# Performance work log

Hardware: AMD Instinct MI355X
Metric: run time of the kernel (lower is better)

The kernel has to match this reference:

```python
import jax, jax.numpy as jnp
import numpy as np

GAMMA = 2          # relu(cos_sim)**gamma, from init gamma=2
EPS = 1e-8         # torch CosineSimilarity eps (norm clamp)
B, C, H, WID = 4, 256, 64, 64


def setup_inputs() -> dict:
    key = jax.random.key(0)
    kx, kw = jax.random.split(key)
    x = jax.random.normal(kx, (B, C, H, WID), dtype=jnp.float32)
    # 1x1 conv (nlayers=1): weight [C_out, C_in], bias [C_out]
    W = jax.random.normal(kw, (C, C), dtype=jnp.float32) * 0.02
    b = jnp.zeros((C,), dtype=jnp.float32)
    return {"x": x, "W": W, "b": b}


def reference(x, W, b):
    # x: [B,C,H,W]. Flatten pixels: p/q index (h*W+w).
    Bs, Cs, Hs, Ws = x.shape
    xf = x.reshape(Bs, Cs, Hs * Ws)                      # [B,C,P]
    norm = jnp.sqrt(jnp.sum(xf * xf, axis=1, keepdims=True))
    xn = xf / jnp.maximum(norm, EPS)                     # channel-normalized
    # full pairwise cosine similarity over pixels, relu, power gamma
    s = jax.nn.relu(jnp.einsum('bcp,bcq->bpq', xn, xn)) ** GAMMA  # [B,P,Q]
    # transform: 1x1 conv = per-pixel linear map over channels
    gx = jnp.einsum('oc,bcp->bop', W, xf) + b[None, :, None]      # [B,C,P]
    # y[b,c,p] = sum_q s[b,p,q] * gx[b,c,q]  (== 'bijhw,bchw->bcij')
    y = jnp.einsum('bpq,bcq->bcp', s, gx)
    return y.reshape(Bs, Cs, Hs, Ws)
```

## Files before the change

kernel.cpp:

```cpp
#include <hip/hip_runtime.h>

#define BN 4
#define CN 256
#define PN 4096
#define QT 64
#define TSTR 264

typedef __attribute__((ext_vector_type(8))) short short8;
typedef __attribute__((ext_vector_type(8))) unsigned short ushort8;
typedef __attribute__((ext_vector_type(4))) float f32x4;
typedef __attribute__((ext_vector_type(2))) unsigned int u32x2;
typedef unsigned int u32;

__device__ __forceinline__ unsigned short f2bf(float f) {
  u32 u = __builtin_bit_cast(u32, f);
  return (unsigned short)((u + 0x7fffu + ((u >> 16) & 1u)) >> 16);
}

__device__ __forceinline__ void async_copy16(const void* g, void* l) {
  __builtin_amdgcn_global_load_lds((const __attribute__((address_space(1))) u32*)g,
                                   (__attribute__((address_space(3))) u32*)l, 16, 0, 0);
}

__global__ __launch_bounds__(256) void k_nx(const float* __restrict__ x,
                                            float* __restrict__ mnorm,
                                            unsigned short* __restrict__ xnT) {
  __shared__ unsigned short tl[64 * TSTR];
  __shared__ float red[4][64];
  const int b = blockIdx.y, p0 = blockIdx.x * 64;
  const int tid = threadIdx.x;
  const int tp = tid & 63, cg = tid >> 6;
  const float* xp = x + ((size_t)b * CN + cg * 64) * PN + p0 + tp;
  float v[64];
  float ss = 0.f;
#pragma unroll
  for (int i = 0; i < 64; ++i) {
    v[i] = xp[(size_t)i * PN];
    ss += v[i] * v[i];
  }
  red[cg][tp] = ss;
  __syncthreads();
  float nrm = sqrtf(red[0][tp] + red[1][tp] + red[2][tp] + red[3][tp]);
  float mn = fmaxf(nrm, 1e-8f);
  float rn = 1.f / mn;
  if (cg == 0) mnorm[b * PN + p0 + tp] = mn;
  unsigned int* tl32 = (unsigned int*)tl;
#pragma unroll
  for (int j = 0; j < 32; ++j) {
    unsigned int w = (unsigned int)f2bf(v[2 * j] * rn) |
                     ((unsigned int)f2bf(v[2 * j + 1] * rn) << 16);
    tl32[tp * (TSTR / 2) + cg * 32 + j] = w;
  }
  __syncthreads();
  unsigned short* xd = xnT + ((size_t)b * PN + p0) * CN;
  const int row = tid >> 2, qc = tid & 3;
#pragma unroll
  for (int i = 0; i < 8; ++i) {
    ushort8 o = *(const ushort8*)(tl + row * TSTR + i * 32 + qc * 8);
    *(ushort8*)(xd + (size_t)row * CN + i * 32 + qc * 8) = o;
  }
}

__global__ void k_gx(const float* __restrict__ Wm, const float* __restrict__ bias,
                     const unsigned short* __restrict__ xnT, const float* __restrict__ mnorm,
                     unsigned short* __restrict__ gxv) {
  int b = blockIdx.z;
  int m0 = blockIdx.y * 64;
  int q0 = blockIdx.x * 64;
  int tid = threadIdx.x;
  int wave = tid >> 6, lane = tid & 63;
  int lr = lane & 15, g = lane >> 4;

  short8 af[8];
  {
    const float* wr = Wm + (size_t)(m0 + wave * 16 + lr) * CN;
#pragma unroll
    for (int k = 0; k < 8; ++k) {
      const float* ap = wr + k * 32 + g * 8;
      short8 a;
#pragma unroll
      for (int j = 0; j < 8; ++j) a[j] = (short)f2bf(ap[j]);
      af[k] = a;
    }
  }
  f32x4 acc[4];
#pragma unroll
  for (int n = 0; n < 4; ++n) acc[n] = (f32x4){0.f, 0.f, 0.f, 0.f};

  const unsigned short* xb = xnT + (size_t)b * PN * CN;
#pragma unroll
  for (int n = 0; n < 4; ++n) {
    const unsigned short* bp = xb + (size_t)(q0 + n * 16 + lr) * CN + g * 8;
#pragma unroll
    for (int k = 0; k < 8; ++k) {
      short8 bf = *(const short8*)(bp + k * 32);
      acc[n] = __builtin_amdgcn_mfma_f32_16x16x32_bf16(af[k], bf, acc[n], 0, 0, 0);
    }
  }
#pragma unroll
  for (int n = 0; n < 4; ++n) {
    int q = q0 + n * 16 + lr;
    float mn = mnorm[b * PN + q];
#pragma unroll
    for (int i = 0; i < 4; ++i) {
      int c = m0 + wave * 16 + g * 4 + i;
      float v = acc[n][i] * mn + bias[c];
      gxv[((size_t)b * CN + c) * PN + q] = f2bf(v);
    }
  }
}

extern __shared__ char smem[];

__global__ __launch_bounds__(512, 2) void k_attn(const unsigned short* __restrict__ xnT,
                                                 const unsigned short* __restrict__ gxv,
                                                 float* __restrict__ d0, float* __restrict__ d1,
                                                 float* __restrict__ d2, float* __restrict__ d3,
                                                 int lq, int ntiles) {
  const int fid = blockIdx.x;
  const int b = fid & 3;
  const int qs = (fid >> 2) & ((1 << lq) - 1);
  const int pblk = fid >> (2 + lq);
  const int tid = threadIdx.x;
  const int wave = tid >> 6, lane = tid & 63, lr = lane & 15, g = lane >> 4;
  const int qbase = qs * (PN >> lq);
  const int p0 = pblk * 256 + wave * 32;
  float* dst = (qs == 0) ? d0 : (qs == 1) ? d1 : (qs == 2) ? d2 : d3;

  const char* xbc = (const char*)xnT + (size_t)b * PN * 512;
  const char* vbc = (const char*)gxv + (size_t)b * CN * PN * 2;

  const int kofs = (lane & 15) * 512 + (lane >> 4) * 16 + wave * 64;
  const int vofs = wave * 131072 + (lane & 15) * 8192 + (lane >> 4) * 16;
  const int ldst = tid * 16;
  const int lane16 = lane * 16;
  const int swb = lr * 16 + (g >> 1) * 256 + (g & 1) * 8;

  auto issue_K = [&](int t) {
    char* kb = smem + (t & 1) * 65536;
    const char* kg = xbc + (size_t)(qbase + t * QT) * 512 + kofs;
#pragma unroll
    for (int j = 0; j < 4; ++j) async_copy16(kg + j * 8192, kb + ldst + j * 8192);
  };
  auto issue_V = [&](int t) {
    char* vb = smem + (t & 1) * 65536 + 32768;
    const char* vg = vbc + (size_t)(qbase + t * QT) * 2 + vofs;
    async_copy16(vg, vb + ldst);
    async_copy16(vg + 1048576, vb + ldst + 8192);
    async_copy16(vg + 64, vb + ldst + 16384);
    async_copy16(vg + 1048576 + 64, vb + ldst + 24576);
  };

  issue_K(0);
  issue_V(0);

  short8 qf[2][8];
#pragma unroll
  for (int mt = 0; mt < 2; ++mt) {
    const char* qp = xbc + (size_t)(p0 + mt * 16 + lr) * 512 + g * 16;
#pragma unroll
    for (int k = 0; k < 8; ++k) qf[mt][k] = *(const short8*)(qp + k * 64);
  }

  f32x4 yacc[2][16];
#pragma unroll
  for (int mt = 0; mt < 2; ++mt)
#pragma unroll
    for (int n = 0; n < 16; ++n) yacc[mt][n] = (f32x4){0.f, 0.f, 0.f, 0.f};

  char* Sme = smem + 131072 + wave * 4096;
  char* Sw = Sme + swb;

  for (int t = 0; t < ntiles; ++t) {
    const char* kb = smem + (t & 1) * 65536;
    const char* vb = kb + 32768;
    asm volatile("s_waitcnt vmcnt(4)" ::: "memory");
    __builtin_amdgcn_s_barrier();
    if (t + 1 < ntiles) issue_K(t + 1);

    f32x4 sacc[4][2];
#pragma unroll
    for (int nt = 0; nt < 4; ++nt)
#pragma unroll
      for (int mt = 0; mt < 2; ++mt) sacc[nt][mt] = (f32x4){0.f, 0.f, 0.f, 0.f};
    __builtin_amdgcn_s_setprio(1);
#pragma unroll
    for (int nh = 0; nh < 2; ++nh) {
#pragma unroll
      for (int k = 0; k < 8; ++k) {
        short8 kf0 = *(const short8*)(kb + ((2 * nh) * 8 + k) * 1024 + lane16);
        short8 kf1 = *(const short8*)(kb + ((2 * nh + 1) * 8 + k) * 1024 + lane16);
        sacc[2 * nh][0] = __builtin_amdgcn_mfma_f32_16x16x32_bf16(kf0, qf[0][k], sacc[2 * nh][0], 0, 0, 0);
        sacc[2 * nh][1] = __builtin_amdgcn_mfma_f32_16x16x32_bf16(kf0, qf[1][k], sacc[2 * nh][1], 0, 0, 0);
        sacc[2 * nh + 1][0] = __builtin_amdgcn_mfma_f32_16x16x32_bf16(kf1, qf[0][k], sacc[2 * nh + 1][0], 0, 0, 0);
        sacc[2 * nh + 1][1] = __builtin_amdgcn_mfma_f32_16x16x32_bf16(kf1, qf[1][k], sacc[2 * nh + 1][1], 0, 0, 0);
      }
    }
    __builtin_amdgcn_s_setprio(0);

#pragma unroll
    for (int nt = 0; nt < 4; ++nt)
#pragma unroll
      for (int mt = 0; mt < 2; ++mt) {
        f32x4 s = sacc[nt][mt];
        float a0 = fmaxf(s[0], 0.f); a0 *= a0;
        float a1 = fmaxf(s[1], 0.f); a1 *= a1;
        float a2 = fmaxf(s[2], 0.f); a2 *= a2;
        float a3 = fmaxf(s[3], 0.f); a3 *= a3;
        u32x2 w;
        asm("v_cvt_pk_bf16_f32 %0, %1, %2" : "=v"(w[0]) : "v"(a0), "v"(a1));
        asm("v_cvt_pk_bf16_f32 %0, %1, %2" : "=v"(w[1]) : "v"(a2), "v"(a3));
        *(u32x2*)(Sw + mt * 2048 + (nt >> 1) * 1024 + (nt & 1) * 512) = w;
      }

    if (t + 1 < ntiles) {
      asm volatile("s_waitcnt vmcnt(4)" ::: "memory");
    } else {
      asm volatile("s_waitcnt vmcnt(0)" ::: "memory");
    }
    __builtin_amdgcn_s_barrier();
    if (t + 1 < ntiles) issue_V(t + 1);

#pragma unroll
    for (int kk = 0; kk < 2; ++kk) {
      short8 pa0 = *(const short8*)(Sme + kk * 1024 + lane16);
      short8 pa1 = *(const short8*)(Sme + 2048 + kk * 1024 + lane16);
      __builtin_amdgcn_s_setprio(1);
#pragma unroll
      for (int n2 = 0; n2 < 16; ++n2) {
        short8 vf = *(const short8*)(vb + (kk * 16 + n2) * 1024 + lane16);
        yacc[0][n2] = __builtin_amdgcn_mfma_f32_16x16x32_bf16(pa0, vf, yacc[0][n2], 0, 0, 0);
        yacc[1][n2] = __builtin_amdgcn_mfma_f32_16x16x32_bf16(pa1, vf, yacc[1][n2], 0, 0, 0);
      }
      __builtin_amdgcn_s_setprio(0);
    }
  }
  __builtin_amdgcn_s_barrier();

  float* yl = (float*)(smem + wave * 16384);
  const int row8 = lane >> 3, p4 = (lane & 7) << 2;
#pragma unroll
  for (int cc = 0; cc < 4; ++cc) {
#pragma unroll
    for (int nn = 0; nn < 4; ++nn)
#pragma unroll
      for (int mt = 0; mt < 2; ++mt)
#pragma unroll
        for (int i = 0; i < 4; ++i)
          yl[(nn * 16 + lr) * 33 + mt * 16 + g * 4 + i] = yacc[mt][cc * 4 + nn][i];
#pragma unroll
    for (int r2 = 0; r2 < 8; ++r2) {
      int c = r2 * 8 + row8;
      float4 v = *(const float4*)(yl + c * 33 + p4);
      *(float4*)(dst + ((size_t)b * CN + cc * 64 + c) * PN + p0 + p4) = v;
    }
  }
}

__global__ void k_add(float* __restrict__ o, const float* __restrict__ a,
                      const float* __restrict__ bb, const float* __restrict__ c,
                      int np, int n4) {
  int i = blockIdx.x * blockDim.x + threadIdx.x;
  int stride = gridDim.x * blockDim.x;
  float4* o4 = (float4*)o;
  const float4* a4 = (const float4*)a;
  const float4* b4 = (const float4*)bb;
  const float4* c4 = (const float4*)c;
  for (; i < n4; i += stride) {
    float4 r = o4[i];
    float4 va = a4[i];
    r.x += va.x; r.y += va.y; r.z += va.z; r.w += va.w;
    if (np > 1) {
      float4 vb = b4[i];
      r.x += vb.x; r.y += vb.y; r.z += vb.z; r.w += vb.w;
      float4 vc = c4[i];
      r.x += vc.x; r.y += vc.y; r.z += vc.z; r.w += vc.w;
    }
    o4[i] = r;
  }
}

extern "C" void kernel_launch(void* const* d_in, const int* in_sizes, int n_in,
                              void* d_out, int out_size, void* d_ws, size_t ws_size,
                              hipStream_t stream) {
  const float* x = (const float*)d_in[0];
  const float* Wm = (const float*)d_in[1];
  const float* bias = (const float*)d_in[2];
  float* out = (float*)d_out;

  char* ws = (char*)d_ws;
  unsigned short* xnT = (unsigned short*)ws;
  unsigned short* gxv = (unsigned short*)(ws + (size_t)8388608);
  float* mnorm = (float*)(ws + (size_t)16777216);
  float* yp0 = (float*)(ws + (size_t)16842752);
  float* yp1 = yp0 + 4194304;
  float* yp2 = yp1 + 4194304;
  const size_t need4 = 16842752ULL + 3ULL * 16777216ULL;

  hipFuncSetAttribute(reinterpret_cast<const void*>(k_attn),
                      hipFuncAttributeMaxDynamicSharedMemorySize, 163840);

  k_nx<<<dim3(PN / 64, BN), 256, 0, stream>>>(x, mnorm, xnT);
  k_gx<<<dim3(PN / 64, CN / 64, BN), 256, 0, stream>>>(Wm, bias, xnT, mnorm, gxv);
  if (ws_size >= need4) {
    k_attn<<<dim3(256), 512, 163840, stream>>>(xnT, gxv, out, yp0, yp1, yp2, 2, (PN / 4) / QT);
    k_add<<<dim3(1024), 256, 0, stream>>>(out, yp0, yp1, yp2, 3, BN * CN * PN / 4);
  } else {
    k_attn<<<dim3(128), 512, 163840, stream>>>(xnT, gxv, out, yp0, yp0, yp0, 1, (PN / 2) / QT);
    k_add<<<dim3(1024), 256, 0, stream>>>(out, yp0, yp0, yp0, 1, BN * CN * PN / 4);
  }
}
```

Before: 114.2 us.

## Split tile loop into barrier-separated phases batching LDS loads before MFMAs

Restructures the per-tile QK and PV loops into four sub-phases each. Each phase first batches its LDS fragment loads into registers, then hits a workgroup barrier, then runs a burst of MFMAs. The next tile's K/V async copies are issued mid-phase rather than at the tile start. The intent is to separate LDS read traffic from MFMA execution across waves, ping-pong style, and to overlap global prefetch better. In exchange it adds several extra barriers per tile and keeps more fragments live in registers, which may cost sync stalls or occupancy.

```diff
diff --git a/kernel.cpp b/kernel.cpp
--- a/kernel.cpp
+++ b/kernel.cpp
@@ -174,63 +174,75 @@
   for (int t = 0; t < ntiles; ++t) {
     const char* kb = smem + (t & 1) * 65536;
     const char* vb = kb + 32768;
-    asm volatile("s_waitcnt vmcnt(4)" ::: "memory");
-    __builtin_amdgcn_s_barrier();
-    if (t + 1 < ntiles) issue_K(t + 1);
-
-    f32x4 sacc[4][2];
-#pragma unroll
-    for (int nt = 0; nt < 4; ++nt)
-#pragma unroll
-      for (int mt = 0; mt < 2; ++mt) sacc[nt][mt] = (f32x4){0.f, 0.f, 0.f, 0.f};
-    __builtin_amdgcn_s_setprio(1);
-#pragma unroll
-    for (int nh = 0; nh < 2; ++nh) {
+
+#pragma unroll
+    for (int nt = 0; nt < 4; ++nt) {
+      if (nt == 0) {
+        asm volatile("s_waitcnt vmcnt(4)" ::: "memory");
+        __builtin_amdgcn_s_barrier();
+      }
+      short8 kf[8];
+#pragma unroll
+      for (int k = 0; k < 8; ++k)
+        kf[k] = *(const short8*)(kb + (nt * 8 + k) * 1024 + lane16);
+      if (nt == 2 && t + 1 < ntiles) issue_K(t + 1);
+      __builtin_amdgcn_s_barrier();
+      f32x4 s0 = (f32x4){0.f, 0.f, 0.f, 0.f}, s1 = (f32x4){0.f, 0.f, 0.f, 0.f};
+      __builtin_amdgcn_s_setprio(1);
 #pragma unroll
       for (int k = 0; k < 8; ++k) {
-        short8 kf0 = *(const short8*)(kb + ((2 * nh) * 8 + k) * 1024 + lane16);
-        short8 kf1 = *(const short8*)(kb + ((2 * nh + 1) * 8 + k) * 1024 + lane16);
-        sacc[2 * nh][0] = __builtin_amdgcn_mfma_f32_16x16x32_bf16(kf0, qf[0][k], sacc[2 * nh][0], 0, 0, 0);
-        sacc[2 * nh][1] = __builtin_amdgcn_mfma_f32_16x16x32_bf16(kf0, qf[1][k], sacc[2 * nh][1], 0, 0, 0);
-        sacc[2 * nh + 1][0] = __builtin_amdgcn_mfma_f32_16x16x32_bf16(kf1, qf[0][k], sacc[2 * nh + 1][0], 0, 0, 0);
-        sacc[2 * nh + 1][1] = __builtin_amdgcn_mfma_f32_16x16x32_bf16(kf1, qf[1][k], sacc[2 * nh + 1][1], 0, 0, 0);
-      }
-    }
-    __builtin_amdgcn_s_setprio(0);
-
-#pragma unroll
-    for (int nt = 0; nt < 4; ++nt)
-#pragma unroll
-      for (int mt = 0; mt < 2; ++mt) {
-        f32x4 s = sacc[nt][mt];
-        float a0 = fmaxf(s[0], 0.f); a0 *= a0;
-        float a1 = fmaxf(s[1], 0.f); a1 *= a1;
-        float a2 = fmaxf(s[2], 0.f); a2 *= a2;
-        float a3 = fmaxf(s[3], 0.f); a3 *= a3;
+        s0 = __builtin_amdgcn_mfma_f32_16x16x32_bf16(kf[k], qf[0][k], s0, 0, 0, 0);
+        s1 = __builtin_amdgcn_mfma_f32_16x16x32_bf16(kf[k], qf[1][k], s1, 0, 0, 0);
+      }
+      __builtin_amdgcn_s_setprio(0);
+      {
+        float a0 = fmaxf(s0[0], 0.f); a0 *= a0;
+        float a1 = fmaxf(s0[1], 0.f); a1 *= a1;
+        float a2 = fmaxf(s0[2], 0.f); a2 *= a2;
+        float a3 = fmaxf(s0[3], 0.f); a3 *= a3;
         u32x2 w;
         asm("v_cvt_pk_bf16_f32 %0, %1, %2" : "=v"(w[0]) : "v"(a0), "v"(a1));
         asm("v_cvt_pk_bf16_f32 %0, %1, %2" : "=v"(w[1]) : "v"(a2), "v"(a3));
-        *(u32x2*)(Sw + mt * 2048 + (nt >> 1) * 1024 + (nt & 1) * 512) = w;
-      }
-
-    if (t + 1 < ntiles) {
-      asm volatile("s_waitcnt vmcnt(4)" ::: "memory");
-    } else {
-      asm volatile("s_waitcnt vmcnt(0)" ::: "memory");
-    }
-    __builtin_amdgcn_s_barrier();
-    if (t + 1 < ntiles) issue_V(t + 1);
-
-#pragma unroll
-    for (int kk = 0; kk < 2; ++kk) {
-      short8 pa0 = *(const short8*)(Sme + kk * 1024 + lane16);
-      short8 pa1 = *(const short8*)(Sme + 2048 + kk * 1024 + lane16);
+        *(u32x2*)(Sw + (nt >> 1) * 1024 + (nt & 1) * 512) = w;
+        float b0 = fmaxf(s1[0], 0.f); b0 *= b0;
+        float b1 = fmaxf(s1[1], 0.f); b1 *= b1;
+        float b2 = fmaxf(s1[2], 0.f); b2 *= b2;
+        float b3 = fmaxf(s1[3], 0.f); b3 *= b3;
+        u32x2 w2;
+        asm("v_cvt_pk_bf16_f32 %0, %1, %2" : "=v"(w2[0]) : "v"(b0), "v"(b1));
+        asm("v_cvt_pk_bf16_f32 %0, %1, %2" : "=v"(w2[1]) : "v"(b2), "v"(b3));
+        *(u32x2*)(Sw + 2048 + (nt >> 1) * 1024 + (nt & 1) * 512) = w2;
+      }
+    }
+
+    short8 pa0, pa1;
+#pragma unroll
+    for (int ph = 0; ph < 4; ++ph) {
+      const int kk = ph >> 1, hf = ph & 1;
+      if (ph == 0) {
+        if (t + 1 < ntiles) {
+          asm volatile("s_waitcnt vmcnt(4)" ::: "memory");
+        } else {
+          asm volatile("s_waitcnt vmcnt(0)" ::: "memory");
+        }
+        __builtin_amdgcn_s_barrier();
+      }
+      if (hf == 0) {
+        pa0 = *(const short8*)(Sme + kk * 1024 + lane16);
+        pa1 = *(const short8*)(Sme + 2048 + kk * 1024 + lane16);
+      }
+      short8 vf[8];
+#pragma unroll
+      for (int j = 0; j < 8; ++j)
+        vf[j] = *(const short8*)(vb + (kk * 16 + hf * 8 + j) * 1024 + lane16);
+      if (ph == 2 && t + 1 < ntiles) issue_V(t + 1);
+      __builtin_amdgcn_s_barrier();
       __builtin_amdgcn_s_setprio(1);
 #pragma unroll
-      for (int n2 = 0; n2 < 16; ++n2) {
-        short8 vf = *(const short8*)(vb + (kk * 16 + n2) * 1024 + lane16);
-        yacc[0][n2] = __builtin_amdgcn_mfma_f32_16x16x32_bf16(pa0, vf, yacc[0][n2], 0, 0, 0);
-        yacc[1][n2] = __builtin_amdgcn_mfma_f32_16x16x32_bf16(pa1, vf, yacc[1][n2], 0, 0, 0);
+      for (int j = 0; j < 8; ++j) {
+        const int n2 = hf * 8 + j;
+        yacc[0][n2] = __builtin_amdgcn_mfma_f32_16x16x32_bf16(pa0, vf[j], yacc[0][n2], 0, 0, 0);
+        yacc[1][n2] = __builtin_amdgcn_mfma_f32_16x16x32_bf16(pa1, vf[j], yacc[1][n2], 0, 0, 0);
       }
       __builtin_amdgcn_s_setprio(0);
     }
```

Result: no change. 116.4 us (+1.9%).

## Pre-swizzle K/V into MFMA fragment layout and keep S in registers

Applied to the files above, without the earlier changes.

The producer kernels now write normalized x and gx in a tiled layout that matches the MFMA fragment order. The attention kernel's async LDS copies become contiguous 16-byte streams, and the Q fragments load directly. The S tile is no longer staged through shared memory: the relu-squared, bf16-packed scores stay in registers and are used as the A operand of the second MFMA, which removes an LDS round trip and cuts dynamic LDS from 160KB to 128KB. The V prefetch is now issued together with K at the top of each iteration, and the wait count changes to match. This relies on the accumulator register layout lining up exactly with the A-operand layout the second MFMA expects.

```diff
diff --git a/kernel.cpp b/kernel.cpp
--- a/kernel.cpp
+++ b/kernel.cpp
@@ -9,7 +9,7 @@
 typedef __attribute__((ext_vector_type(8))) short short8;
 typedef __attribute__((ext_vector_type(8))) unsigned short ushort8;
 typedef __attribute__((ext_vector_type(4))) float f32x4;
-typedef __attribute__((ext_vector_type(2))) unsigned int u32x2;
+typedef __attribute__((ext_vector_type(4))) unsigned int u32x4;
 typedef unsigned int u32;
 
 __device__ __forceinline__ unsigned short f2bf(float f) {
@@ -22,12 +22,13 @@
                                    (__attribute__((address_space(3))) u32*)l, 16, 0, 0);
 }
 
+
 __global__ __launch_bounds__(256) void k_nx(const float* __restrict__ x,
                                             float* __restrict__ mnorm,
-                                            unsigned short* __restrict__ xnT) {
+                                            unsigned short* __restrict__ xnK) {
   __shared__ unsigned short tl[64 * TSTR];
   __shared__ float red[4][64];
-  const int b = blockIdx.y, p0 = blockIdx.x * 64;
+  const int b = blockIdx.y, qb = blockIdx.x, p0 = qb * 64;
   const int tid = threadIdx.x;
   const int tp = tid & 63, cg = tid >> 6;
   const float* xp = x + ((size_t)b * CN + cg * 64) * PN + p0 + tp;
@@ -52,24 +53,27 @@
     tl32[tp * (TSTR / 2) + cg * 32 + j] = w;
   }
   __syncthreads();
-  unsigned short* xd = xnT + ((size_t)b * PN + p0) * CN;
-  const int row = tid >> 2, qc = tid & 3;
-#pragma unroll
-  for (int i = 0; i < 8; ++i) {
-    ushort8 o = *(const ushort8*)(tl + row * TSTR + i * 32 + qc * 8);
-    *(ushort8*)(xd + (size_t)row * CN + i * 32 + qc * 8) = o;
+  char* dstb = (char*)xnK + (size_t)b * (PN * CN * 2) + (size_t)qb * 32768;
+#pragma unroll
+  for (int m = 0; m < 8; ++m) {
+    int idx = m * 256 + tid;
+    int F = idx >> 6, ln = idx & 63;
+    int pl = (F >> 3) * 16 + (ln & 15);
+    int ch = (F & 7) * 32 + (ln >> 4) * 8;
+    ushort8 o = *(const ushort8*)(tl + pl * TSTR + ch);
+    *(ushort8*)(dstb + (size_t)idx * 16) = o;
   }
 }
 
 __global__ void k_gx(const float* __restrict__ Wm, const float* __restrict__ bias,
-                     const unsigned short* __restrict__ xnT, const float* __restrict__ mnorm,
-                     unsigned short* __restrict__ gxv) {
-  int b = blockIdx.z;
-  int m0 = blockIdx.y * 64;
-  int q0 = blockIdx.x * 64;
-  int tid = threadIdx.x;
-  int wave = tid >> 6, lane = tid & 63;
-  int lr = lane & 15, g = lane >> 4;
+                     const unsigned short* __restrict__ xnK, const float* __restrict__ mnorm,
+                     unsigned short* __restrict__ gxF) {
+  const int b = blockIdx.z;
+  const int m0 = blockIdx.y * 64;
+  const int qb = blockIdx.x, q0 = qb * 64;
+  const int tid = threadIdx.x;
+  const int wave = tid >> 6, lane = tid & 63;
+  const int lr = lane & 15, g = lane >> 4;
 
   short8 af[8];
   {
@@ -87,33 +91,36 @@
 #pragma unroll
   for (int n = 0; n < 4; ++n) acc[n] = (f32x4){0.f, 0.f, 0.f, 0.f};
 
-  const unsigned short* xb = xnT + (size_t)b * PN * CN;
-#pragma unroll
-  for (int n = 0; n < 4; ++n) {
-    const unsigned short* bp = xb + (size_t)(q0 + n * 16 + lr) * CN + g * 8;
+  const char* xb = (const char*)xnK + (size_t)b * (PN * CN * 2) + (size_t)qb * 32768;
+#pragma unroll
+  for (int n = 0; n < 4; ++n)
 #pragma unroll
     for (int k = 0; k < 8; ++k) {
-      short8 bf = *(const short8*)(bp + k * 32);
+      short8 bf = *(const short8*)(xb + ((n * 8 + k) << 10) + ((g * 16 + lr) << 4));
       acc[n] = __builtin_amdgcn_mfma_f32_16x16x32_bf16(af[k], bf, acc[n], 0, 0, 0);
     }
-  }
+  char* vbb = (char*)gxF + (size_t)b * (PN * CN * 2) + (size_t)qb * 32768;
 #pragma unroll
   for (int n = 0; n < 4; ++n) {
     int q = q0 + n * 16 + lr;
     float mn = mnorm[b * PN + q];
+    int kk = n >> 1;
+    int q32 = (n & 1) * 16 + lr;
+    int gp = (q32 >> 2) & 3;
+    int j = ((q32 >> 4) & 1) * 4 + (q32 & 3);
 #pragma unroll
     for (int i = 0; i < 4; ++i) {
       int c = m0 + wave * 16 + g * 4 + i;
       float v = acc[n][i] * mn + bias[c];
-      gxv[((size_t)b * CN + c) * PN + q] = f2bf(v);
+      *(unsigned short*)(vbb + ((kk * 16 + (c >> 4)) << 10) + (gp << 8) + ((c & 15) << 4) + (j << 1)) = f2bf(v);
     }
   }
 }
 
 extern __shared__ char smem[];
 
-__global__ __launch_bounds__(512, 2) void k_attn(const unsigned short* __restrict__ xnT,
-                                                 const unsigned short* __restrict__ gxv,
+__global__ __launch_bounds__(512, 2) void k_attn(const unsigned short* __restrict__ xnK,
+                                                 const unsigned short* __restrict__ gxF,
                                                  float* __restrict__ d0, float* __restrict__ d1,
                                                  float* __restrict__ d2, float* __restrict__ d3,
                                                  int lq, int ntiles) {
@@ -123,43 +130,43 @@
   const int pblk = fid >> (2 + lq);
   const int tid = threadIdx.x;
   const int wave = tid >> 6, lane = tid & 63, lr = lane & 15, g = lane >> 4;
-  const int qbase = qs * (PN >> lq);
+  const int qb0 = (qs * (PN >> lq)) >> 6;
   const int p0 = pblk * 256 + wave * 32;
   float* dst = (qs == 0) ? d0 : (qs == 1) ? d1 : (qs == 2) ? d2 : d3;
 
-  const char* xbc = (const char*)xnT + (size_t)b * PN * 512;
-  const char* vbc = (const char*)gxv + (size_t)b * CN * PN * 2;
-
-  const int kofs = (lane & 15) * 512 + (lane >> 4) * 16 + wave * 64;
-  const int vofs = wave * 131072 + (lane & 15) * 8192 + (lane >> 4) * 16;
+  const char* xb = (const char*)xnK + (size_t)b * (PN * CN * 2);
+  const char* vg = (const char*)gxF + (size_t)b * (PN * CN * 2);
+  const char* kq = xb + (size_t)qb0 * 32768;
+  const char* vq = vg + (size_t)qb0 * 32768;
   const int ldst = tid * 16;
   const int lane16 = lane * 16;
-  const int swb = lr * 16 + (g >> 1) * 256 + (g & 1) * 8;
 
   auto issue_K = [&](int t) {
     char* kb = smem + (t & 1) * 65536;
-    const char* kg = xbc + (size_t)(qbase + t * QT) * 512 + kofs;
-#pragma unroll
-    for (int j = 0; j < 4; ++j) async_copy16(kg + j * 8192, kb + ldst + j * 8192);
+    const char* s = kq + (size_t)t * 32768 + ldst;
+#pragma unroll
+    for (int j = 0; j < 4; ++j) async_copy16(s + j * 8192, kb + ldst + j * 8192);
   };
   auto issue_V = [&](int t) {
     char* vb = smem + (t & 1) * 65536 + 32768;
-    const char* vg = vbc + (size_t)(qbase + t * QT) * 2 + vofs;
-    async_copy16(vg, vb + ldst);
-    async_copy16(vg + 1048576, vb + ldst + 8192);
-    async_copy16(vg + 64, vb + ldst + 16384);
-    async_copy16(vg + 1048576 + 64, vb + ldst + 24576);
+    const char* s = vq + (size_t)t * 32768 + ldst;
+#pragma unroll
+    for (int j = 0; j < 4; ++j) async_copy16(s + j * 8192, vb + ldst + j * 8192);
   };
 
   issue_K(0);
   issue_V(0);
 
   short8 qf[2][8];
-#pragma unroll
-  for (int mt = 0; mt < 2; ++mt) {
-    const char* qp = xbc + (size_t)(p0 + mt * 16 + lr) * 512 + g * 16;
-#pragma unroll
-    for (int k = 0; k < 8; ++k) qf[mt][k] = *(const short8*)(qp + k * 64);
+  {
+    const char* qpb = xb + (size_t)(pblk * 4 + (wave >> 1)) * 32768;
+#pragma unroll
+    for (int mt = 0; mt < 2; ++mt) {
+      int ntp = (wave & 1) * 2 + mt;
+#pragma unroll
+      for (int k = 0; k < 8; ++k)
+        qf[mt][k] = *(const short8*)(qpb + ((ntp * 8 + k) << 10) + ((g * 16 + lr) << 4));
+    }
   }
 
   f32x4 yacc[2][16];
@@ -167,70 +174,69 @@
   for (int mt = 0; mt < 2; ++mt)
 #pragma unroll
     for (int n = 0; n < 16; ++n) yacc[mt][n] = (f32x4){0.f, 0.f, 0.f, 0.f};
-
-  char* Sme = smem + 131072 + wave * 4096;
-  char* Sw = Sme + swb;
 
   for (int t = 0; t < ntiles; ++t) {
     const char* kb = smem + (t & 1) * 65536;
     const char* vb = kb + 32768;
+
     asm volatile("s_waitcnt vmcnt(4)" ::: "memory");
     __builtin_amdgcn_s_barrier();
-    if (t + 1 < ntiles) issue_K(t + 1);
-
-    f32x4 sacc[4][2];
-#pragma unroll
-    for (int nt = 0; nt < 4; ++nt)
-#pragma unroll
-      for (int mt = 0; mt < 2; ++mt) sacc[nt][mt] = (f32x4){0.f, 0.f, 0.f, 0.f};
-    __builtin_amdgcn_s_setprio(1);
+    if (t + 1 < ntiles) { issue_K(t + 1); issue_V(t + 1); }
+
+    u32 pa[2][2][4];
 #pragma unroll
     for (int nh = 0; nh < 2; ++nh) {
+      f32x4 sacc[2][2];
+#pragma unroll
+      for (int n0 = 0; n0 < 2; ++n0)
+#pragma unroll
+        for (int mt = 0; mt < 2; ++mt) sacc[n0][mt] = (f32x4){0.f, 0.f, 0.f, 0.f};
+      __builtin_amdgcn_s_setprio(1);
 #pragma unroll
       for (int k = 0; k < 8; ++k) {
         short8 kf0 = *(const short8*)(kb + ((2 * nh) * 8 + k) * 1024 + lane16);
         short8 kf1 = *(const short8*)(kb + ((2 * nh + 1) * 8 + k) * 1024 + lane16);
-        sacc[2 * nh][0] = __builtin_amdgcn_mfma_f32_16x16x32_bf16(kf0, qf[0][k], sacc[2 * nh][0], 0, 0, 0);
-        sacc[2 * nh][1] = __builtin_amdgcn_mfma_f32_16x16x32_bf16(kf0, qf[1][k], sacc[2 * nh][1], 0, 0, 0);
-        sacc[2 * nh + 1][0] = __builtin_amdgcn_mfma_f32_16x16x32_bf16(kf1, qf[0][k], sacc[2 * nh + 1][0], 0, 0, 0);
-        sacc[2 * nh + 1][1] = __builtin_amdgcn_mfma_f32_16x16x32_bf16(kf1, qf[1][k], sacc[2 * nh + 1][1], 0, 0, 0);
+        sacc[0][0] = __builtin_amdgcn_mfma_f32_16x16x32_bf16(kf0, qf[0][k], sacc[0][0], 0, 0, 0);
+        sacc[0][1] = __builtin_amdgcn_mfma_f32_16x16x32_bf16(kf0, qf[1][k], sacc[0][1], 0, 0, 0);
+        sacc[1][0] = __builtin_amdgcn_mfma_f32_16x16x32_bf16(kf1, qf[0][k], sacc[1][0], 0, 0, 0);
+        sacc[1][1] = __builtin_amdgcn_mfma_f32_16x16x32_bf16(kf1, qf[1][k], sacc[1][1], 0, 0, 0);
       }
-    }
-    __builtin_amdgcn_s_setprio(0);
-
-#pragma unroll
-    for (int nt = 0; nt < 4; ++nt)
-#pragma unroll
-      for (int mt = 0; mt < 2; ++mt) {
-        f32x4 s = sacc[nt][mt];
-        float a0 = fmaxf(s[0], 0.f); a0 *= a0;
-        float a1 = fmaxf(s[1], 0.f); a1 *= a1;
-        float a2 = fmaxf(s[2], 0.f); a2 *= a2;
-        float a3 = fmaxf(s[3], 0.f); a3 *= a3;
-        u32x2 w;
-        asm("v_cvt_pk_bf16_f32 %0, %1, %2" : "=v"(w[0]) : "v"(a0), "v"(a1));
-        asm("v_cvt_pk_bf16_f32 %0, %1, %2" : "=v"(w[1]) : "v"(a2), "v"(a3));
-        *(u32x2*)(Sw + mt * 2048 + (nt >> 1) * 1024 + (nt & 1) * 512) = w;
-      }
+      __builtin_amdgcn_s_setprio(0);
+#pragma unroll
+      for (int mt = 0; mt < 2; ++mt)
+#pragma unroll
+        for (int n0 = 0; n0 < 2; ++n0)
+#pragma unroll
+          for (int h = 0; h < 2; ++h) {
+            float a0 = fmaxf(sacc[n0][mt][2 * h], 0.f);
+            a0 *= a0;
+            float a1 = fmaxf(sacc[n0][mt][2 * h + 1], 0.f);
+            a1 *= a1;
+            u32 w;
+            asm("v_cvt_pk_bf16_f32 %0, %1, %2" : "=v"(w) : "v"(a0), "v"(a1));
+            pa[mt][nh][n0 * 2 + h] = w;
+          }
+    }
 
     if (t + 1 < ntiles) {
-      asm volatile("s_waitcnt vmcnt(4)" ::: "memory");
+      asm volatile("s_waitcnt vmcnt(8)" ::: "memory");
     } else {
       asm volatile("s_waitcnt vmcnt(0)" ::: "memory");
     }
     __builtin_amdgcn_s_barrier();
-    if (t + 1 < ntiles) issue_V(t + 1);
 
 #pragma unroll
     for (int kk = 0; kk < 2; ++kk) {
-      short8 pa0 = *(const short8*)(Sme + kk * 1024 + lane16);
-      short8 pa1 = *(const short8*)(Sme + 2048 + kk * 1024 + lane16);
+      u32x4 w0 = {pa[0][kk][0], pa[0][kk][1], pa[0][kk][2], pa[0][kk][3]};
+      u32x4 w1 = {pa[1][kk][0], pa[1][kk][1], pa[1][kk][2], pa[1][kk][3]};
+      short8 a0 = __builtin_bit_cast(short8, w0);
+      short8 a1 = __builtin_bit_cast(short8, w1);
       __builtin_amdgcn_s_setprio(1);
 #pragma unroll
       for (int n2 = 0; n2 < 16; ++n2) {
         short8 vf = *(const short8*)(vb + (kk * 16 + n2) * 1024 + lane16);
-        yacc[0][n2] = __builtin_amdgcn_mfma_f32_16x16x32_bf16(pa0, vf, yacc[0][n2], 0, 0, 0);
-        yacc[1][n2] = __builtin_amdgcn_mfma_f32_16x16x32_bf16(pa1, vf, yacc[1][n2], 0, 0, 0);
+        yacc[0][n2] = __builtin_amdgcn_mfma_f32_16x16x32_bf16(a0, vf, yacc[0][n2], 0, 0, 0);
+        yacc[1][n2] = __builtin_amdgcn_mfma_f32_16x16x32_bf16(a1, vf, yacc[1][n2], 0, 0, 0);
       }
       __builtin_amdgcn_s_setprio(0);
     }
@@ -289,8 +295,8 @@
   float* out = (float*)d_out;
 
   char* ws = (char*)d_ws;
-  unsigned short* xnT = (unsigned short*)ws;
-  unsigned short* gxv = (unsigned short*)(ws + (size_t)8388608);
+  unsigned short* xnK = (unsigned short*)ws;
+  unsigned short* gxF = (unsigned short*)(ws + (size_t)8388608);
   float* mnorm = (float*)(ws + (size_t)16777216);
   float* yp0 = (float*)(ws + (size_t)16842752);
   float* yp1 = yp0 + 4194304;
@@ -298,15 +304,15 @@
   const size_t need4 = 16842752ULL + 3ULL * 16777216ULL;
 
   hipFuncSetAttribute(reinterpret_cast<const void*>(k_attn),
-                      hipFuncAttributeMaxDynamicSharedMemorySize, 163840);
-
-  k_nx<<<dim3(PN / 64, BN), 256, 0, stream>>>(x, mnorm, xnT);
-  k_gx<<<dim3(PN / 64, CN / 64, BN), 256, 0, stream>>>(Wm, bias, xnT, mnorm, gxv);
+                      hipFuncAttributeMaxDynamicSharedMemorySize, 131072);
+
+  k_nx<<<dim3(PN / 64, BN), 256, 0, stream>>>(x, mnorm, xnK);
+  k_gx<<<dim3(PN / 64, CN / 64, BN), 256, 0, stream>>>(Wm, bias, xnK, mnorm, gxF);
   if (ws_size >= need4) {
-    k_attn<<<dim3(256), 512, 163840, stream>>>(xnT, gxv, out, yp0, yp1, yp2, 2, (PN / 4) / QT);
+    k_attn<<<dim3(256), 512, 131072, stream>>>(xnK, gxF, out, yp0, yp1, yp2, 2, (PN / 4) / QT);
     k_add<<<dim3(1024), 256, 0, stream>>>(out, yp0, yp1, yp2, 3, BN * CN * PN / 4);
   } else {
-    k_attn<<<dim3(128), 512, 163840, stream>>>(xnT, gxv, out, yp0, yp0, yp0, 1, (PN / 2) / QT);
+    k_attn<<<dim3(128), 512, 131072, stream>>>(xnK, gxF, out, yp0, yp0, yp0, 1, (PN / 2) / QT);
     k_add<<<dim3(1024), 256, 0, stream>>>(out, yp0, yp0, yp0, 1, BN * CN * PN / 4);
   }
 }
```

Result: faster. 101.1 us (-11.5%).
